# Kernel optimization log

Hardware: AMD Instinct MI355X
Metric: run time of the kernel (lower is better)

Reference implementation:

```python
import jax, jax.numpy as jnp
import numpy as np

B, S, D, H = 4, 2048, 1024, 16
HD = D // H
EPS = 1e-5


def setup_inputs() -> dict:
    key = jax.random.key(0)
    ks = jax.random.split(key, 12)
    scale = 1.0 / np.sqrt(D)
    inp = {
        "x": jax.random.normal(ks[0], (B, S, D), dtype=jnp.float32),
        "template_ids": jax.random.randint(ks[1], (B, S), 0, 1000, dtype=jnp.int64)
            if jax.config.jax_enable_x64 else jax.random.randint(ks[1], (B, S), 0, 1000, dtype=jnp.int32),
        "attention_mask": jnp.ones((B, S), dtype=jnp.int32),
        "Wq": jax.random.normal(ks[2], (D, D), dtype=jnp.float32) * scale,
        "bq": jnp.zeros((D,), dtype=jnp.float32),
        "Wk": jax.random.normal(ks[3], (D, D), dtype=jnp.float32) * scale,
        "bk": jnp.zeros((D,), dtype=jnp.float32),
        "Wv": jax.random.normal(ks[4], (D, D), dtype=jnp.float32) * scale,
        "bv": jnp.zeros((D,), dtype=jnp.float32),
        "Wo": jax.random.normal(ks[5], (D, D), dtype=jnp.float32) * scale,
        "bo": jnp.zeros((D,), dtype=jnp.float32),
        "gamma": jnp.ones((D,), dtype=jnp.float32),
        "beta": jnp.zeros((D,), dtype=jnp.float32),
    }
    return inp


def _split_heads(t):
    # [B,S,D] -> [B,H,S,HD]
    return t.reshape(B, S, H, HD).transpose(0, 2, 1, 3)


def reference(x, template_ids, attention_mask, Wq, bq, Wk, bk, Wv, bv, Wo, bo, gamma, beta):
    q = _split_heads(x @ Wq.T + bq)
    k = _split_heads(x @ Wk.T + bk)
    v = _split_heads(x @ Wv.T + bv)
    # [B,H,S,S]
    scores = jnp.einsum("bhqd,bhkd->bhqk", q, k) / jnp.sqrt(jnp.float32(HD))
    mask = attention_mask[:, None, None, :]  # broadcast over heads and query dim
    scores = jnp.where(mask == 0, jnp.float32(-10000.0), scores)
    attn = jax.nn.softmax(scores, axis=-1)  # dropout is identity in eval
    out = jnp.einsum("bhqk,bhkd->bhqd", attn, v)
    out = out.transpose(0, 2, 1, 3).reshape(B, S, D)
    out = out @ Wo.T + bo
    # residual + LayerNorm
    y = x + out
    mu = jnp.mean(y, axis=-1, keepdims=True)
    var = jnp.var(y, axis=-1, keepdims=True)
    return (y - mu) * jax.lax.rsqrt(var + EPS) * gamma + beta
```

## Files before the change

kernel.cpp:

```cpp
#include <hip/hip_runtime.h>

typedef unsigned short u16;
typedef unsigned int u32;
typedef __attribute__((ext_vector_type(8))) short bf16x8;
typedef __attribute__((ext_vector_type(4))) float f32x4;

#define NB 4
#define SS 2048
#define DD 1024
#define NH 16
#define HD 64
#define MM (NB*SS)

struct __align__(16) Pack16 { unsigned int w0, w1, w2, w3; };
union PU { Pack16 p; u16 s[8]; };

__device__ __forceinline__ float b2f(u16 u) {
    union { unsigned int i; float f; } v; v.i = ((unsigned int)u) << 16; return v.f;
}
__device__ __forceinline__ u16 f2b(float f) {
    union { unsigned int i; float f; } v; v.f = f;
    return (u16)((v.i + 0x7FFFu + ((v.i >> 16) & 1u)) >> 16);
}
__device__ __forceinline__ u32 packbf(float a, float b) {
    u32 ia = __float_as_uint(a), ib = __float_as_uint(b);
    return ((ia + 0x8000u) >> 16) | ((ib + 0x8000u) & 0xFFFF0000u);
}
__device__ __forceinline__ float rdS(const void* p, size_t i, int mode) {
    return mode ? ((const float*)p)[i] : b2f(((const u16*)p)[i]);
}

__device__ __forceinline__ void cp16(const u16* g, u16* l) {
    __builtin_amdgcn_global_load_lds(
        (const __attribute__((address_space(1))) void*)g,
        (__attribute__((address_space(3))) void*)l, 16, 0, 0);
}

__global__ void detect_kernel(const unsigned int* __restrict__ gamma_w, int* __restrict__ mode) {
    *mode = (gamma_w[0] == 0x3F800000u) ? 1 : 0;
}

#define GX ((size_t)MM * DD / 8)
#define GW ((size_t)DD * DD / 8)
#define GTOT (GX + 4 * GW + 512)

__global__ __launch_bounds__(256) void convert_kernel(
    const void* __restrict__ x,
    const void* __restrict__ Wq, const void* __restrict__ Wk,
    const void* __restrict__ Wv, const void* __restrict__ Wo,
    const void* __restrict__ bq, const void* __restrict__ bk,
    const void* __restrict__ bv, const void* __restrict__ bo,
    u16* __restrict__ xb, u16* __restrict__ Wc, u16* __restrict__ Wob,
    u16* __restrict__ bcat, const int* __restrict__ modep)
{
    const int mode = *modep;
    size_t g = (size_t)blockIdx.x * 256 + threadIdx.x;
    const void* src; u16* dst; size_t off; float sc = 1.0f;
    if (g < GX)               { src = x;  dst = xb;              off = g * 8; }
    else if (g < GX + GW)     { src = Wq; dst = Wc;              off = (g - GX) * 8; sc = 0.125f; }
    else if (g < GX + 2 * GW) { src = Wk; dst = Wc + (size_t)DD * DD;     off = (g - GX - GW) * 8; }
    else if (g < GX + 3 * GW) { src = Wv; dst = Wc + (size_t)2 * DD * DD; off = (g - GX - 2 * GW) * 8; }
    else if (g < GX + 4 * GW) { src = Wo; dst = Wob;             off = (g - GX - 3 * GW) * 8; }
    else {
        size_t gg = g - (GX + 4 * GW);
        int which = (int)(gg >> 7); off = (gg & 127) * 8;
        src = (which == 0) ? bq : (which == 1) ? bk : (which == 2) ? bv : bo;
        dst = bcat + which * DD;
        if (which == 0) sc = 0.125f;
    }
    PU o;
    if (mode) {
        const float* s = (const float*)src + off;
        float4 a = ((const float4*)s)[0];
        float4 b = ((const float4*)s)[1];
        o.s[0] = f2b(a.x * sc); o.s[1] = f2b(a.y * sc);
        o.s[2] = f2b(a.z * sc); o.s[3] = f2b(a.w * sc);
        o.s[4] = f2b(b.x * sc); o.s[5] = f2b(b.y * sc);
        o.s[6] = f2b(b.z * sc); o.s[7] = f2b(b.w * sc);
    } else {
        PU in; in.p = *(const Pack16*)((const u16*)src + off);
#pragma unroll
        for (int j = 0; j < 8; j++) o.s[j] = f2b(b2f(in.s[j]) * sc);
    }
    *(Pack16*)(dst + off) = o.p;
}

__global__ __launch_bounds__(256) void gemm_qkv(
    const u16* __restrict__ xb, const u16* __restrict__ Wc, const u16* __restrict__ bcat,
    u16* __restrict__ Q, u16* __restrict__ K, u16* __restrict__ V)
{
    __shared__ __align__(16) u16 As[128 * 64];
    __shared__ __align__(16) u16 Bs[128 * 64];

    const int tid  = threadIdx.x;
    const int wv   = tid >> 6;
    const int lane = tid & 63;
    const int wy = wv >> 1, wx = wv & 1;
    const int l15 = lane & 15, quad = lane >> 4;
    const int m0 = blockIdx.x * 128, n0 = blockIdx.y * 128;
    const int srow = lane >> 3;
    const int sw   = ((lane & 7) ^ srow) * 8;
    const int key  = l15 & 7;

    f32x4 acc[4][4];
#pragma unroll
    for (int i = 0; i < 4; i++)
#pragma unroll
        for (int j = 0; j < 4; j++) acc[i][j] = (f32x4){0.f, 0.f, 0.f, 0.f};

    for (int k0 = 0; k0 < DD; k0 += 64) {
#pragma unroll
        for (int c = 0; c < 4; c++) {
            cp16(&xb[(size_t)(m0 + wv * 32 + c * 8 + srow) * DD + k0 + sw],
                 &As[wv * 2048 + c * 512]);
            cp16(&Wc[(size_t)(n0 + wv * 32 + c * 8 + srow) * DD + k0 + sw],
                 &Bs[wv * 2048 + c * 512]);
        }
        __syncthreads();
#pragma unroll
        for (int ks = 0; ks < 2; ks++) {
            bf16x8 a[4], bb[4];
#pragma unroll
            for (int mt = 0; mt < 4; mt++)
                a[mt] = *(const bf16x8*)&As[(wy * 64 + mt * 16 + l15) * 64 +
                                            (((ks << 2) + quad) ^ key) * 8];
#pragma unroll
            for (int nt = 0; nt < 4; nt++)
                bb[nt] = *(const bf16x8*)&Bs[(wx * 64 + nt * 16 + l15) * 64 +
                                             (((ks << 2) + quad) ^ key) * 8];
#pragma unroll
            for (int mt = 0; mt < 4; mt++)
#pragma unroll
                for (int nt = 0; nt < 4; nt++)
                    acc[mt][nt] = __builtin_amdgcn_mfma_f32_16x16x32_bf16(
                        a[mt], bb[nt], acc[mt][nt], 0, 0, 0);
        }
        __syncthreads();
    }

    const int z = (n0 + wx * 64) >> 10;
    u16* out = (z == 0) ? Q : (z == 1) ? K : V;
#pragma unroll
    for (int nt = 0; nt < 4; nt++) {
        int n_g = n0 + wx * 64 + nt * 16 + l15;
        float bv_ = b2f(bcat[n_g]);
        int nn = n_g & 1023;
        int h = nn >> 6, hd = nn & 63;
#pragma unroll
        for (int mt = 0; mt < 4; mt++) {
#pragma unroll
            for (int r = 0; r < 4; r++) {
                int m_g = m0 + wy * 64 + mt * 16 + quad * 4 + r;
                int b = m_g >> 11, s = m_g & (SS - 1);
                u16 val = f2b(acc[mt][nt][r] + bv_);
                if (z == 2)
                    out[((size_t)(b * NH + h) * HD + hd) * SS + s] = val;
                else
                    out[(((size_t)(b * NH + h) * SS) + s) * HD + hd] = val;
            }
        }
    }
}

__global__ __launch_bounds__(256) void attn_kernel(
    const u16* __restrict__ Q, const u16* __restrict__ K, const u16* __restrict__ V,
    const int* __restrict__ mask, u16* __restrict__ O)
{
    const int bh = blockIdx.y;
    const int b = bh >> 4, h = bh & 15;
    const int q0 = blockIdx.x * 128;
    const u16* Qp  = Q + (size_t)bh * SS * HD;
    const u16* Kp  = K + (size_t)bh * SS * HD;
    const u16* Vtg = V + (size_t)bh * HD * SS;
    const int* mk = mask + b * SS;

    __shared__ __align__(16) u16 Kl[64 * 64];
    __shared__ __align__(16) u16 Vt[64 * 64];

    const int tid  = threadIdx.x;
    const int w    = tid >> 6;
    const int lane = tid & 63;
    const int l15 = lane & 15, quad = lane >> 4;
    const int srow = lane >> 3;
    const int sw   = ((lane & 7) ^ srow) * 8;
    const int key  = l15 & 7;

    bf16x8 qf[2][2];
#pragma unroll
    for (int qt = 0; qt < 2; qt++)
#pragma unroll
        for (int ks = 0; ks < 2; ks++)
            qf[qt][ks] = *(const bf16x8*)&Qp[(size_t)(q0 + w * 32 + qt * 16 + l15) * HD +
                                             ks * 32 + quad * 8];

    f32x4 oacc[2][4];
#pragma unroll
    for (int i = 0; i < 2; i++)
#pragma unroll
        for (int j = 0; j < 4; j++) oacc[i][j] = (f32x4){0.f, 0.f, 0.f, 0.f};

    float lsum[2] = {0.f, 0.f};

    const int laneA = (quad & 1) * 32 + l15;
    const int laneB = laneA + 16;
    const bool hi = (quad >> 1) != 0;

    for (int kv0 = 0; kv0 < SS; kv0 += 64) {
#pragma unroll
        for (int c = 0; c < 2; c++) {
            cp16(&Kp[(size_t)(kv0 + w * 16 + c * 8 + srow) * HD + sw],
                 &Kl[w * 1024 + c * 512]);
            cp16(&Vtg[(size_t)(w * 16 + c * 8 + srow) * SS + kv0 + sw],
                 &Vt[w * 1024 + c * 512]);
        }
        int mv = mk[kv0 + lane];
        bool anymask = (__ballot(mv == 0) != 0ull);
        __syncthreads();

        f32x4 sacc[4][2];
#pragma unroll
        for (int i = 0; i < 4; i++)
#pragma unroll
            for (int j = 0; j < 2; j++) sacc[i][j] = (f32x4){0.f, 0.f, 0.f, 0.f};
#pragma unroll
        for (int ks = 0; ks < 2; ks++) {
            bf16x8 kf[4];
#pragma unroll
            for (int kvt = 0; kvt < 4; kvt++)
                kf[kvt] = *(const bf16x8*)&Kl[(kvt * 16 + l15) * 64 +
                                              (((ks << 2) + quad) ^ key) * 8];
#pragma unroll
            for (int kvt = 0; kvt < 4; kvt++)
#pragma unroll
                for (int qt = 0; qt < 2; qt++)
                    sacc[kvt][qt] = __builtin_amdgcn_mfma_f32_16x16x32_bf16(
                        kf[kvt], qf[qt][ks], sacc[kvt][qt], 0, 0, 0);
        }

        u32 pw[4][2][2];
#pragma unroll
        for (int kvt = 0; kvt < 4; kvt++)
#pragma unroll
            for (int qt = 0; qt < 2; qt++) {
                f32x4 vv = sacc[kvt][qt];
                if (anymask) {
#pragma unroll
                    for (int r = 0; r < 4; r++) {
                        int kv = kv0 + kvt * 16 + quad * 4 + r;
                        if (mk[kv] == 0) vv[r] = -10000.0f;
                    }
                }
                float p0 = __expf(vv[0]);
                float p1 = __expf(vv[1]);
                float p2 = __expf(vv[2]);
                float p3 = __expf(vv[3]);
                lsum[qt] += (p0 + p1) + (p2 + p3);
                pw[kvt][qt][0] = packbf(p0, p1);
                pw[kvt][qt][1] = packbf(p2, p3);
            }

#pragma unroll
        for (int ks2 = 0; ks2 < 2; ks2++) {
            bf16x8 vf[4];
#pragma unroll
            for (int nt = 0; nt < 4; nt++)
                vf[nt] = *(const bf16x8*)&Vt[(nt * 16 + l15) * 64 +
                                             (((ks2 << 2) + quad) ^ key) * 8];
            const int t0 = 2 * ks2, t1 = 2 * ks2 + 1;
#pragma unroll
            for (int qt = 0; qt < 2; qt++) {
                u32 a0 = (u32)__shfl((int)pw[t0][qt][0], laneA, 64);
                u32 b0 = (u32)__shfl((int)pw[t1][qt][0], laneA, 64);
                u32 a1 = (u32)__shfl((int)pw[t0][qt][1], laneA, 64);
                u32 b1 = (u32)__shfl((int)pw[t1][qt][1], laneA, 64);
                u32 a2 = (u32)__shfl((int)pw[t0][qt][0], laneB, 64);
                u32 b2 = (u32)__shfl((int)pw[t1][qt][0], laneB, 64);
                u32 a3 = (u32)__shfl((int)pw[t0][qt][1], laneB, 64);
                u32 b3 = (u32)__shfl((int)pw[t1][qt][1], laneB, 64);
                union { u32 u[4]; bf16x8 v; } af;
                af.u[0] = hi ? b0 : a0;
                af.u[1] = hi ? b1 : a1;
                af.u[2] = hi ? b2 : a2;
                af.u[3] = hi ? b3 : a3;
#pragma unroll
                for (int nt = 0; nt < 4; nt++)
                    oacc[qt][nt] = __builtin_amdgcn_mfma_f32_16x16x32_bf16(
                        af.v, vf[nt], oacc[qt][nt], 0, 0, 0);
            }
        }
        __syncthreads();
    }

#pragma unroll
    for (int qt = 0; qt < 2; qt++) {
        lsum[qt] += __shfl_xor(lsum[qt], 16, 64);
        lsum[qt] += __shfl_xor(lsum[qt], 32, 64);
    }
#pragma unroll
    for (int qt = 0; qt < 2; qt++) {
#pragma unroll
        for (int r = 0; r < 4; r++) {
            float inv = 1.0f / __shfl(lsum[qt], quad * 4 + r, 64);
            int row = q0 + w * 32 + qt * 16 + quad * 4 + r;
            size_t base = ((size_t)(b * SS + row)) * DD + h * HD;
#pragma unroll
            for (int nt = 0; nt < 4; nt++)
                O[base + nt * 16 + l15] = f2b(oacc[qt][nt][r] * inv);
        }
    }
}

__global__ __launch_bounds__(256) void gemm_oproj(
    const u16* __restrict__ A, const u16* __restrict__ Wob, const u16* __restrict__ bcat,
    u16* __restrict__ Y)
{
    __shared__ __align__(16) u16 As[128 * 64];
    __shared__ __align__(16) u16 Bs[128 * 64];

    const int tid  = threadIdx.x;
    const int wv   = tid >> 6;
    const int lane = tid & 63;
    const int wy = wv >> 1, wx = wv & 1;
    const int l15 = lane & 15, quad = lane >> 4;
    const int m0 = blockIdx.x * 128, n0 = blockIdx.y * 128;
    const int srow = lane >> 3;
    const int sw   = ((lane & 7) ^ srow) * 8;
    const int key  = l15 & 7;

    f32x4 acc[4][4];
#pragma unroll
    for (int i = 0; i < 4; i++)
#pragma unroll
        for (int j = 0; j < 4; j++) acc[i][j] = (f32x4){0.f, 0.f, 0.f, 0.f};

    for (int k0 = 0; k0 < DD; k0 += 64) {
#pragma unroll
        for (int c = 0; c < 4; c++) {
            cp16(&A[(size_t)(m0 + wv * 32 + c * 8 + srow) * DD + k0 + sw],
                 &As[wv * 2048 + c * 512]);
            cp16(&Wob[(size_t)(n0 + wv * 32 + c * 8 + srow) * DD + k0 + sw],
                 &Bs[wv * 2048 + c * 512]);
        }
        __syncthreads();
#pragma unroll
        for (int ks = 0; ks < 2; ks++) {
            bf16x8 a[4], bb[4];
#pragma unroll
            for (int mt = 0; mt < 4; mt++)
                a[mt] = *(const bf16x8*)&As[(wy * 64 + mt * 16 + l15) * 64 +
                                            (((ks << 2) + quad) ^ key) * 8];
#pragma unroll
            for (int nt = 0; nt < 4; nt++)
                bb[nt] = *(const bf16x8*)&Bs[(wx * 64 + nt * 16 + l15) * 64 +
                                             (((ks << 2) + quad) ^ key) * 8];
#pragma unroll
            for (int mt = 0; mt < 4; mt++)
#pragma unroll
                for (int nt = 0; nt < 4; nt++)
                    acc[mt][nt] = __builtin_amdgcn_mfma_f32_16x16x32_bf16(
                        a[mt], bb[nt], acc[mt][nt], 0, 0, 0);
        }
        __syncthreads();
    }

#pragma unroll
    for (int nt = 0; nt < 4; nt++) {
        int n_g = n0 + wx * 64 + nt * 16 + l15;
        float bv_ = b2f(bcat[3 * DD + n_g]);
#pragma unroll
        for (int mt = 0; mt < 4; mt++) {
#pragma unroll
            for (int r = 0; r < 4; r++) {
                int m_g = m0 + wy * 64 + mt * 16 + quad * 4 + r;
                Y[(size_t)m_g * DD + n_g] = f2b(acc[mt][nt][r] + bv_);
            }
        }
    }
}

__global__ __launch_bounds__(256) void ln_kernel(
    const u16* __restrict__ Yp, const void* __restrict__ x,
    const void* __restrict__ gamma, const void* __restrict__ beta,
    void* __restrict__ out, const int* __restrict__ modep)
{
    const int mode = *modep;
    const int w    = threadIdx.x >> 6;
    const int lane = threadIdx.x & 63;
    const int row  = blockIdx.x * 4 + w;
    const u16* y = Yp + (size_t)row * DD;

    float vals[16];
    float s = 0.f, sq = 0.f;
#pragma unroll
    for (int i = 0; i < 2; i++) {
        PU d; d.p = *(const Pack16*)&y[i * 512 + lane * 8];
        if (mode) {
            const float* xp = (const float*)x + (size_t)row * DD + i * 512 + lane * 8;
            float4 xa = ((const float4*)xp)[0];
            float4 xb2 = ((const float4*)xp)[1];
            float xr[8] = {xa.x, xa.y, xa.z, xa.w, xb2.x, xb2.y, xb2.z, xb2.w};
#pragma unroll
            for (int j = 0; j < 8; j++) {
                float f = b2f(d.s[j]) + xr[j];
                vals[i * 8 + j] = f;
                s += f; sq += f * f;
            }
        } else {
            const u16* xp = (const u16*)x + (size_t)row * DD + i * 512 + lane * 8;
            PU xd; xd.p = *(const Pack16*)xp;
#pragma unroll
            for (int j = 0; j < 8; j++) {
                float f = b2f(d.s[j]) + b2f(xd.s[j]);
                vals[i * 8 + j] = f;
                s += f; sq += f * f;
            }
        }
    }
#pragma unroll
    for (int off = 1; off < 64; off <<= 1) {
        s  += __shfl_xor(s, off);
        sq += __shfl_xor(sq, off);
    }
    float mu  = s * (1.0f / 1024.0f);
    float var = sq * (1.0f / 1024.0f) - mu * mu;
    float rs  = rsqrtf(var + 1e-5f);

#pragma unroll
    for (int i = 0; i < 2; i++) {
        float r8[8];
#pragma unroll
        for (int j = 0; j < 8; j++) {
            int col = i * 512 + lane * 8 + j;
            r8[j] = (vals[i * 8 + j] - mu) * rs * rdS(gamma, col, mode) + rdS(beta, col, mode);
        }
        if (mode) {
            float* of = (float*)out + (size_t)row * DD + i * 512 + lane * 8;
            ((float4*)of)[0] = make_float4(r8[0], r8[1], r8[2], r8[3]);
            ((float4*)of)[1] = make_float4(r8[4], r8[5], r8[6], r8[7]);
        } else {
            PU ob;
#pragma unroll
            for (int j = 0; j < 8; j++) ob.s[j] = f2b(r8[j]);
            *(Pack16*)((u16*)out + (size_t)row * DD + i * 512 + lane * 8) = ob.p;
        }
    }
}

extern "C" void kernel_launch(void* const* d_in, const int* in_sizes, int n_in,
                              void* d_out, int out_size, void* d_ws, size_t ws_size,
                              hipStream_t stream)
{
    const void* x     = d_in[0];
    const int* mask   = (const int*)d_in[2];
    const void* Wq    = d_in[3];
    const void* bq    = d_in[4];
    const void* Wk    = d_in[5];
    const void* bk    = d_in[6];
    const void* Wv    = d_in[7];
    const void* bv    = d_in[8];
    const void* Wo    = d_in[9];
    const void* bo    = d_in[10];
    const void* gamma = d_in[11];
    const void* beta  = d_in[12];

    int* modep = (int*)d_ws;
    const size_t n = (size_t)MM * DD;
    u16* xb   = (u16*)((char*)d_ws + 256);
    u16* Wc   = xb + n;
    u16* Wob  = Wc + (size_t)3 * DD * DD;
    u16* bcat = Wob + (size_t)DD * DD;
    u16* Qb   = bcat + 4096;
    u16* Kb   = Qb + n;
    u16* Vb   = Kb + n;
    u16* Ab   = Vb + n;
    u16* Yb   = xb;

    detect_kernel<<<1, 1, 0, stream>>>((const unsigned int*)gamma, modep);
    convert_kernel<<<(unsigned)(GTOT / 256), 256, 0, stream>>>(
        x, Wq, Wk, Wv, Wo, bq, bk, bv, bo, xb, Wc, Wob, bcat, modep);
    gemm_qkv<<<dim3(MM / 128, 3 * DD / 128), 256, 0, stream>>>(xb, Wc, bcat, Qb, Kb, Vb);
    attn_kernel<<<dim3(SS / 128, NB * NH), 256, 0, stream>>>(Qb, Kb, Vb, mask, Ab);
    gemm_oproj<<<dim3(MM / 128, DD / 128), 256, 0, stream>>>(Ab, Wob, bcat, Yb);
    ln_kernel<<<MM / 4, 256, 0, stream>>>(Yb, x, gamma, beta, d_out, modep);
}
```

Before: 393.4 us.

## Use exp2 with log2e-folded Q scale and LDS staging for P fragments

Folds log2(e) into the Q weight/bias scale so the softmax can use the native exp2 instruction instead of __expf. It also replaces the eight cross-lane shuffles per P fragment with a per-wave padded LDS staging buffer that is written after exp and read back as bf16x8 MFMA operands. The mask fill value is doubled to stay equivalent in base 2, and launch bounds now request 3 blocks per CU. The trade is extra LDS footprint and LDS write/read traffic in exchange for fewer shuffle and VALU operations, plus some register-pressure risk from the occupancy hint.

```diff
diff --git a/kernel.cpp b/kernel.cpp
--- a/kernel.cpp
+++ b/kernel.cpp
@@ -29,6 +29,7 @@
 __device__ __forceinline__ float rdS(const void* p, size_t i, int mode) {
     return mode ? ((const float*)p)[i] : b2f(((const u16*)p)[i]);
 }
+__device__ __forceinline__ float ex2(float x) { return __builtin_amdgcn_exp2f(x); }
 
 __device__ __forceinline__ void cp16(const u16* g, u16* l) {
     __builtin_amdgcn_global_load_lds(
@@ -40,6 +41,7 @@
     *mode = (gamma_w[0] == 0x3F800000u) ? 1 : 0;
 }
 
+#define QSC 0.1803368801111204f
 #define GX ((size_t)MM * DD / 8)
 #define GW ((size_t)DD * DD / 8)
 #define GTOT (GX + 4 * GW + 512)
@@ -57,7 +59,7 @@
     size_t g = (size_t)blockIdx.x * 256 + threadIdx.x;
     const void* src; u16* dst; size_t off; float sc = 1.0f;
     if (g < GX)               { src = x;  dst = xb;              off = g * 8; }
-    else if (g < GX + GW)     { src = Wq; dst = Wc;              off = (g - GX) * 8; sc = 0.125f; }
+    else if (g < GX + GW)     { src = Wq; dst = Wc;              off = (g - GX) * 8; sc = QSC; }
     else if (g < GX + 2 * GW) { src = Wk; dst = Wc + (size_t)DD * DD;     off = (g - GX - GW) * 8; }
     else if (g < GX + 3 * GW) { src = Wv; dst = Wc + (size_t)2 * DD * DD; off = (g - GX - 2 * GW) * 8; }
     else if (g < GX + 4 * GW) { src = Wo; dst = Wob;             off = (g - GX - 3 * GW) * 8; }
@@ -66,7 +68,7 @@
         int which = (int)(gg >> 7); off = (gg & 127) * 8;
         src = (which == 0) ? bq : (which == 1) ? bk : (which == 2) ? bv : bo;
         dst = bcat + which * DD;
-        if (which == 0) sc = 0.125f;
+        if (which == 0) sc = QSC;
     }
     PU o;
     if (mode) {
@@ -162,7 +164,7 @@
     }
 }
 
-__global__ __launch_bounds__(256) void attn_kernel(
+__global__ __launch_bounds__(256, 3) void attn_kernel(
     const u16* __restrict__ Q, const u16* __restrict__ K, const u16* __restrict__ V,
     const int* __restrict__ mask, u16* __restrict__ O)
 {
@@ -176,6 +178,7 @@
 
     __shared__ __align__(16) u16 Kl[64 * 64];
     __shared__ __align__(16) u16 Vt[64 * 64];
+    __shared__ __align__(16) u16 Pw[4 * 32 * 72];
 
     const int tid  = threadIdx.x;
     const int w    = tid >> 6;
@@ -184,6 +187,7 @@
     const int srow = lane >> 3;
     const int sw   = ((lane & 7) ^ srow) * 8;
     const int key  = l15 & 7;
+    u16* Pme = &Pw[w * 2304];
 
     bf16x8 qf[2][2];
 #pragma unroll
@@ -200,10 +204,6 @@
         for (int j = 0; j < 4; j++) oacc[i][j] = (f32x4){0.f, 0.f, 0.f, 0.f};
 
     float lsum[2] = {0.f, 0.f};
-
-    const int laneA = (quad & 1) * 32 + l15;
-    const int laneB = laneA + 16;
-    const bool hi = (quad >> 1) != 0;
 
     for (int kv0 = 0; kv0 < SS; kv0 += 64) {
 #pragma unroll
@@ -237,7 +237,6 @@
                         kf[kvt], qf[qt][ks], sacc[kvt][qt], 0, 0, 0);
         }
 
-        u32 pw[4][2][2];
 #pragma unroll
         for (int kvt = 0; kvt < 4; kvt++)
 #pragma unroll
@@ -247,16 +246,16 @@
 #pragma unroll
                     for (int r = 0; r < 4; r++) {
                         int kv = kv0 + kvt * 16 + quad * 4 + r;
-                        if (mk[kv] == 0) vv[r] = -10000.0f;
+                        if (mk[kv] == 0) vv[r] = -20000.0f;
                     }
                 }
-                float p0 = __expf(vv[0]);
-                float p1 = __expf(vv[1]);
-                float p2 = __expf(vv[2]);
-                float p3 = __expf(vv[3]);
+                float p0 = ex2(vv[0]);
+                float p1 = ex2(vv[1]);
+                float p2 = ex2(vv[2]);
+                float p3 = ex2(vv[3]);
                 lsum[qt] += (p0 + p1) + (p2 + p3);
-                pw[kvt][qt][0] = packbf(p0, p1);
-                pw[kvt][qt][1] = packbf(p2, p3);
+                uint2 wr; wr.x = packbf(p0, p1); wr.y = packbf(p2, p3);
+                *(uint2*)&Pme[(qt * 16 + l15) * 72 + kvt * 16 + quad * 4] = wr;
             }
 
 #pragma unroll
@@ -266,26 +265,14 @@
             for (int nt = 0; nt < 4; nt++)
                 vf[nt] = *(const bf16x8*)&Vt[(nt * 16 + l15) * 64 +
                                              (((ks2 << 2) + quad) ^ key) * 8];
-            const int t0 = 2 * ks2, t1 = 2 * ks2 + 1;
 #pragma unroll
             for (int qt = 0; qt < 2; qt++) {
-                u32 a0 = (u32)__shfl((int)pw[t0][qt][0], laneA, 64);
-                u32 b0 = (u32)__shfl((int)pw[t1][qt][0], laneA, 64);
-                u32 a1 = (u32)__shfl((int)pw[t0][qt][1], laneA, 64);
-                u32 b1 = (u32)__shfl((int)pw[t1][qt][1], laneA, 64);
-                u32 a2 = (u32)__shfl((int)pw[t0][qt][0], laneB, 64);
-                u32 b2 = (u32)__shfl((int)pw[t1][qt][0], laneB, 64);
-                u32 a3 = (u32)__shfl((int)pw[t0][qt][1], laneB, 64);
-                u32 b3 = (u32)__shfl((int)pw[t1][qt][1], laneB, 64);
-                union { u32 u[4]; bf16x8 v; } af;
-                af.u[0] = hi ? b0 : a0;
-                af.u[1] = hi ? b1 : a1;
-                af.u[2] = hi ? b2 : a2;
-                af.u[3] = hi ? b3 : a3;
+                bf16x8 af = *(const bf16x8*)&Pme[(qt * 16 + l15) * 72 +
+                                                 ks2 * 32 + quad * 8];
 #pragma unroll
                 for (int nt = 0; nt < 4; nt++)
                     oacc[qt][nt] = __builtin_amdgcn_mfma_f32_16x16x32_bf16(
-                        af.v, vf[nt], oacc[qt][nt], 0, 0, 0);
+                        af, vf[nt], oacc[qt][nt], 0, 0, 0);
             }
         }
         __syncthreads();
```

Measured after the change: 352.1 us. 10.5% less time.
